# Kernel optimization log

Hardware: AMD Instinct MI355X
Metric: run time of the kernel (lower is better)

## Reference

```python
import jax, jax.numpy as jnp
import numpy as np

B = 8192      # batch
F = 20        # sparse features
V = 1000      # vocab per sparse feature
E = 32        # embedding dim
ND = 10       # dense features
IN0 = (F + ND) * E  # 960 total embed dim
T = 2         # tasks
K = 4         # task experts per task
S = 4         # shared experts
D = 512       # expert dim
H = 256       # tower hidden
TEMP = 2.0    # gate temperature
EPS = 1e-5    # batchnorm eps


def setup_inputs() -> dict:
    key = jax.random.key(0)
    ks = iter(jax.random.split(key, 64))
    n = lambda shape, s=0.02: jax.random.normal(next(ks), shape, dtype=jnp.float32) * s
    inp = {
        'sparse_features': jax.random.randint(next(ks), (B, F), 0, V, dtype=jnp.int32),
        'dense_features': jax.random.normal(next(ks), (B, ND), dtype=jnp.float32),
        'emb_tables': n((F, V, E), 0.05),
        'dense_W': n((ND, ND * E)),
        'dense_b': jnp.zeros((ND * E,), jnp.float32),
    }
    for i, ind in enumerate([IN0, D, D]):
        inp[f'l{i}_Wt'] = n((T, K, ind, D))
        inp[f'l{i}_bt'] = jnp.zeros((T, K, D), jnp.float32)
        inp[f'l{i}_Ws'] = n((S, ind, D))
        inp[f'l{i}_bs'] = jnp.zeros((S, D), jnp.float32)
        inp[f'l{i}_Wg'] = n((T, ind, K + S))
        inp[f'l{i}_bg'] = jnp.zeros((T, K + S), jnp.float32)
    inp['tw1'] = n((T, D, H)); inp['tb1'] = jnp.zeros((T, H), jnp.float32)
    inp['bn_g'] = jnp.ones((T, H), jnp.float32); inp['bn_b'] = jnp.zeros((T, H), jnp.float32)
    inp['bn_m'] = jnp.zeros((T, H), jnp.float32); inp['bn_v'] = jnp.ones((T, H), jnp.float32)
    inp['tw2'] = n((T, H, H // 2)); inp['tb2'] = jnp.zeros((T, H // 2), jnp.float32)
    inp['tw3'] = n((T, H // 2)); inp['tb3'] = jnp.zeros((T,), jnp.float32)
    return inp


def _ple_layer(x, Wt, bt, Ws, bs, Wg, bg):
    # x: [B, in]; Wt: [T,K,in,D]; Ws: [S,in,D]; Wg: [T,in,K+S]
    shared = jax.nn.relu(jnp.einsum('bi,sio->bso', x, Ws) + bs)        # [B,S,D]
    task = jax.nn.relu(jnp.einsum('bi,tkio->btko', x, Wt) + bt)        # [B,T,K,D]
    Bn = x.shape[0]
    stack = jnp.concatenate(
        [task, jnp.broadcast_to(shared[:, None], (Bn, T) + shared.shape[1:])], axis=2)  # [B,T,K+S,D]
    gw = jax.nn.softmax((jnp.einsum('bi,tie->bte', x, Wg) + bg) / TEMP, axis=-1)        # [B,T,K+S]
    return jnp.einsum('bte,bted->btd', gw, stack)                      # [B,T,D]


def reference(sparse_features, dense_features, emb_tables, dense_W, dense_b,
              l0_Wt, l0_bt, l0_Ws, l0_bs, l0_Wg, l0_bg,
              l1_Wt, l1_bt, l1_Ws, l1_bs, l1_Wg, l1_bg,
              l2_Wt, l2_bt, l2_Ws, l2_bs, l2_Wg, l2_bg,
              tw1, tb1, bn_g, bn_b, bn_m, bn_v, tw2, tb2, tw3, tb3):
    # embedding: per-feature table lookup then concat with projected dense
    sp = emb_tables[jnp.arange(F)[None, :], sparse_features]           # [B,F,E]
    embed = jnp.concatenate(
        [sp.reshape(sp.shape[0], F * E), dense_features @ dense_W + dense_b], axis=1)  # [B,IN0]

    x = embed
    tout = None
    for (Wt, bt, Ws, bs, Wg, bg) in [
        (l0_Wt, l0_bt, l0_Ws, l0_bs, l0_Wg, l0_bg),
        (l1_Wt, l1_bt, l1_Ws, l1_bs, l1_Wg, l1_bg),
        (l2_Wt, l2_bt, l2_Ws, l2_bs, l2_Wg, l2_bg),
    ]:
        tout = _ple_layer(x, Wt, bt, Ws, bs, Wg, bg)   # [B,T,D]
        x = tout.mean(axis=1)                           # next layer input

    # task towers (eval mode: BN uses running stats, dropout off)
    h = jnp.einsum('btd,tdh->bth', tout, tw1) + tb1
    h = (h - bn_m) / jnp.sqrt(bn_v + EPS) * bn_g + bn_b
    h = jax.nn.relu(h)
    h = jax.nn.relu(jnp.einsum('bth,thg->btg', h, tw2) + tb2)
    logits = jnp.einsum('btg,tg->bt', h, tw3) + tb3     # [B,T]

    ctr = jax.nn.sigmoid(logits[:, 0])
    cvr_raw = jax.nn.sigmoid(logits[:, 1])
    ctcvr = ctr * cvr_raw
    # use_esmm=True -> cvr_pred == ctcvr
    return jnp.stack([ctr, ctcvr, ctcvr])               # [3,B]: ctr, cvr, ctcvr
```

## Files before the change

kernel.cpp:

```cpp
#include <hip/hip_runtime.h>
#include <math.h>

#define Bn 8192
#define INP0 960
#define Dn 512
#define Hn 256
#define TEMP_INV 0.5f

typedef __attribute__((ext_vector_type(8))) short short8;
typedef __attribute__((ext_vector_type(8))) unsigned short ushort8;
typedef __attribute__((ext_vector_type(4))) float f32x4;
typedef __attribute__((ext_vector_type(2))) long lx2;

__device__ __forceinline__ int swz(int x) { return x ^ ((x >> 3) & 0x70); }

__device__ __forceinline__ unsigned short f2bf(float f) {
  unsigned u = __builtin_bit_cast(unsigned, f);
  u += 0x7FFF + ((u >> 16) & 1);
  return (unsigned short)(u >> 16);
}
__device__ __forceinline__ float bf2f(unsigned short s) {
  unsigned u = ((unsigned)s) << 16;
  return __builtin_bit_cast(float, u);
}
__device__ __forceinline__ int pk4fp8(float a, float b, float c, float d) {
  int r = __builtin_amdgcn_cvt_pk_fp8_f32(a, b, 0, 0);
  r = __builtin_amdgcn_cvt_pk_fp8_f32(c, d, r, 1);
  return r;
}
__device__ __forceinline__ void gload16(const void* g, void* l) {
  __builtin_amdgcn_global_load_lds(
      (const __attribute__((address_space(1))) unsigned int*)g,
      (__attribute__((address_space(3))) unsigned int*)l, 16, 0, 0);
}

#define WBT_L1_OFF 5898240
#define WBT_L2_OFF 9043968

__global__ __launch_bounds__(256) void conv_w_all(
    const float* __restrict__ Wt0, const float* __restrict__ Ws0,
    const float* __restrict__ Wt1, const float* __restrict__ Ws1,
    const float* __restrict__ Wt2, const float* __restrict__ Ws2,
    unsigned char* __restrict__ Wbt) {
  __shared__ float T[64][65];
  int layer = blockIdx.z / 12, e = blockIdx.z - layer * 12;
  int IN = (layer == 0) ? 960 : 512;
  int NK = IN / 64;
  int kk = blockIdx.x;
  if (kk >= NK) return;
  int dblk = blockIdx.y;
  const float* Wtl = (layer == 0) ? Wt0 : (layer == 1) ? Wt1 : Wt2;
  const float* Wsl = (layer == 0) ? Ws0 : (layer == 1) ? Ws1 : Ws2;
  size_t obase = (layer == 0) ? 0 : (layer == 1) ? (size_t)WBT_L1_OFF : (size_t)WBT_L2_OFF;
  int t = threadIdx.x;
  const float* base = (e < 8) ? (Wtl + (size_t)e * IN * Dn) : (Wsl + (size_t)(e - 8) * IN * Dn);
  int k = t >> 2, dg = t & 3;
  const float* gp = base + (size_t)(kk * 64 + k) * Dn + dblk * 64 + dg * 16;
#pragma unroll
  for (int i = 0; i < 4; ++i) {
    float4 v = *(const float4*)(gp + i * 4);
    T[dg * 16 + i * 4 + 0][k] = v.x;
    T[dg * 16 + i * 4 + 1][k] = v.y;
    T[dg * 16 + i * 4 + 2][k] = v.z;
    T[dg * 16 + i * 4 + 3][k] = v.w;
  }
  __syncthreads();
  int col = t >> 2, gq = t & 3;
  int g = gq ^ ((col >> 1) & 3);
  const float* Tc = T[col];
  int4 o;
  o.x = pk4fp8(Tc[g * 8 + 0] * 16.f, Tc[g * 8 + 1] * 16.f, Tc[g * 8 + 2] * 16.f, Tc[g * 8 + 3] * 16.f);
  o.y = pk4fp8(Tc[g * 8 + 4] * 16.f, Tc[g * 8 + 5] * 16.f, Tc[g * 8 + 6] * 16.f, Tc[g * 8 + 7] * 16.f);
  o.z = pk4fp8(Tc[32 + g * 8 + 0] * 16.f, Tc[32 + g * 8 + 1] * 16.f, Tc[32 + g * 8 + 2] * 16.f, Tc[32 + g * 8 + 3] * 16.f);
  o.w = pk4fp8(Tc[32 + g * 8 + 4] * 16.f, Tc[32 + g * 8 + 5] * 16.f, Tc[32 + g * 8 + 6] * 16.f, Tc[32 + g * 8 + 7] * 16.f);
  *(int4*)(Wbt + obase + (((size_t)(dblk * NK + kk) * 12 + e) << 12) + t * 16) = o;
}

__global__ __launch_bounds__(64) void conv_wg_all(
    const float* __restrict__ Wg0, const float* __restrict__ Wg1,
    const float* __restrict__ Wg2, unsigned short* __restrict__ out) {
  int layer = blockIdx.z;
  int IN = (layer == 0) ? 960 : 512;
  int i = blockIdx.x * 64 + threadIdx.x;
  if (i >= IN) return;
  int e = blockIdx.y;
  int t = e >> 3, eg = e & 7;
  const float* Wg = (layer == 0) ? Wg0 : (layer == 1) ? Wg1 : Wg2;
  size_t off = (layer == 0) ? 0 : (layer == 1) ? (size_t)16 * 960 : (size_t)16 * 960 + 16 * 512;
  out[off + (size_t)e * IN + i] = f2bf(Wg[((size_t)t * IN + i) * 8 + eg]);
}

template <int K, int H>
__global__ __launch_bounds__(256) void conv_tw(const float* __restrict__ W,
                                               unsigned short* __restrict__ out) {
  __shared__ float T[64][33];
  int kk = blockIdx.x, hb = blockIdx.y, t = blockIdx.z;
  int tid = threadIdx.x;
  const float* base = W + (size_t)t * K * H;
  int k = tid >> 3, dq = tid & 7;
  const float* gp = base + (size_t)(kk * 32 + k) * H + hb * 64 + dq * 8;
  float4 v0 = *(const float4*)gp, v1 = *(const float4*)(gp + 4);
  T[dq * 8 + 0][k] = v0.x; T[dq * 8 + 1][k] = v0.y; T[dq * 8 + 2][k] = v0.z; T[dq * 8 + 3][k] = v0.w;
  T[dq * 8 + 4][k] = v1.x; T[dq * 8 + 5][k] = v1.y; T[dq * 8 + 6][k] = v1.z; T[dq * 8 + 7][k] = v1.w;
  __syncthreads();
  int L = tid * 16;
  int nat = swz(L);
  int c = nat >> 6, k0 = (nat & 63) >> 1;
  ushort8 o;
#pragma unroll
  for (int u = 0; u < 8; ++u) o[u] = f2bf(T[c][k0 + u]);
  const int NHB = H / 64;
  *(ushort8*)(out + (((size_t)(kk * NHB + hb) * 2 + t) << 11) + (L >> 1)) = o;
}

__global__ __launch_bounds__(256) void embed_kernel(
    const int* __restrict__ sparse, const float* __restrict__ dense,
    const float* __restrict__ emb, const float* __restrict__ dW,
    const float* __restrict__ db, const unsigned short* __restrict__ wgb0,
    const float* __restrict__ bg0,
    unsigned short* __restrict__ xn, unsigned char* __restrict__ xt,
    float* __restrict__ gates) {
  int b0 = blockIdx.x * 4, t = threadIdx.x;
  __shared__ float dfs[4][10];
  __shared__ __align__(16) unsigned short xrow[4][960];
  if (t < 40) dfs[t / 10][t % 10] = dense[(b0 + t / 10) * 10 + t % 10];
  __syncthreads();
  if (t < 240) {
    int c = t * 4;
#pragma unroll 1
    for (int r = 0; r < 4; ++r) {
      int b = b0 + r;
      float v[4];
      if (c < 640) {
        int f = c >> 5, e0 = c & 31;
        int idx = sparse[b * 20 + f];
        const float* ep = emb + ((size_t)f * 1000 + idx) * 32 + e0;
        float4 q = *(const float4*)ep;
        v[0] = q.x; v[1] = q.y; v[2] = q.z; v[3] = q.w;
      } else {
        int j = c - 640;
#pragma unroll
        for (int u = 0; u < 4; ++u) {
          float a = db[j + u];
#pragma unroll
          for (int d = 0; d < 10; ++d) a += dfs[r][d] * dW[d * 320 + j + u];
          v[u] = a;
        }
      }
      ushort4 pk;
      pk.x = f2bf(v[0]); pk.y = f2bf(v[1]); pk.z = f2bf(v[2]); pk.w = f2bf(v[3]);
      *(ushort4*)(xn + (size_t)b * 960 + c) = pk;
      *(ushort4*)(&xrow[r][c]) = pk;
      int col = b & 63;
      int lc = c & 63;
      int ks = lc >> 5, g = (lc & 31) >> 3, j0 = lc & 7;
      int gq = g ^ ((col >> 1) & 3);
      int pos = (col << 6) + (gq << 4) + (ks << 3) + j0;
      int p8 = pk4fp8(v[0] * 16.f, v[1] * 16.f, v[2] * 16.f, v[3] * 16.f);
      *(int*)(xt + (((size_t)(c >> 6) * 128 + (b >> 6)) << 12) + pos) = p8;
    }
  }
  __syncthreads();
  int r = t >> 6, lane = t & 63;
  int e = lane & 15, slice = lane >> 4;
  const unsigned short* xr = &xrow[r][slice * 240];
  const unsigned short* wr = wgb0 + (size_t)e * 960 + slice * 240;
  float p = 0.f;
#pragma unroll 2
  for (int i = 0; i < 240; i += 8) {
    short8 xv = *(const short8*)(xr + i);
    short8 wv2 = *(const short8*)(wr + i);
#pragma unroll
    for (int u = 0; u < 8; ++u)
      p += bf2f((unsigned short)xv[u]) * bf2f((unsigned short)wv2[u]);
  }
  p += __shfl_xor(p, 16);
  p += __shfl_xor(p, 32);
  float z = (p + bg0[e]) * TEMP_INV;
  float m = z;
  m = fmaxf(m, __shfl_xor(m, 1)); m = fmaxf(m, __shfl_xor(m, 2)); m = fmaxf(m, __shfl_xor(m, 4));
  float ex = expf(z - m);
  float s = ex;
  s += __shfl_xor(s, 1); s += __shfl_xor(s, 2); s += __shfl_xor(s, 4);
  if (lane < 16) gates[(size_t)(b0 + r) * 16 + lane] = ex / s;
}

template <int IN>
__global__ __launch_bounds__(256) void gate_kernel(
    const unsigned short* __restrict__ x, const unsigned short* __restrict__ wgb,
    const float* __restrict__ bg, float* __restrict__ gates) {
  int tid = threadIdx.x;
  int wv = tid >> 6, lane = tid & 63;
  int b = blockIdx.x * 4 + wv;
  int e = lane & 15, slice = lane >> 4;
  const unsigned short* xr = x + (size_t)b * IN + slice * (IN / 4);
  const unsigned short* wr = wgb + (size_t)e * IN + slice * (IN / 4);
  float p = 0.f;
#pragma unroll 2
  for (int i = 0; i < IN / 4; i += 8) {
    short8 xv = *(const short8*)(xr + i);
    short8 wv2 = *(const short8*)(wr + i);
#pragma unroll
    for (int u = 0; u < 8; ++u)
      p += bf2f((unsigned short)xv[u]) * bf2f((unsigned short)wv2[u]);
  }
  p += __shfl_xor(p, 16);
  p += __shfl_xor(p, 32);
  int t = e >> 3, eg = e & 7;
  float z = (p + bg[t * 8 + eg]) * TEMP_INV;
  float m = z;
  m = fmaxf(m, __shfl_xor(m, 1)); m = fmaxf(m, __shfl_xor(m, 2)); m = fmaxf(m, __shfl_xor(m, 4));
  float ex = expf(z - m);
  float s = ex;
  s += __shfl_xor(s, 1); s += __shfl_xor(s, 2); s += __shfl_xor(s, 4);
  if (lane < 16) gates[(size_t)b * 16 + lane] = ex / s;
}

#define GSH 0
#define OUTS 4096
#define SB 22528
#define STG 53248

template <int IN, int MODE>
__global__ __launch_bounds__(768, 3) void ple_mfma(
    const unsigned char* __restrict__ xt, const float* __restrict__ gates,
    const unsigned char* __restrict__ Wbt,
    const float* __restrict__ btb, const float* __restrict__ bsh,
    unsigned short* __restrict__ outn, unsigned char* __restrict__ outt8,
    unsigned short* __restrict__ outtb) {
  __shared__ __align__(16) char smem[129024];
  const int NK = IN / 64;
  int tid = threadIdx.x;
  int wv = tid >> 6, lane = tid & 63;
  int r = lane & 15, g = lane >> 4;
  int s = blockIdx.x;
  int dblk = s & 7, bblk = s >> 3;
  int b0 = bblk * 64, d0 = dblk * 64;

  if (tid < 256)
    *(float4*)(smem + GSH + tid * 16) = *(const float4*)(gates + (size_t)b0 * 16 + tid * 4);

  f32x4 acc[4][4];
#pragma unroll
  for (int i = 0; i < 4; ++i)
#pragma unroll
    for (int j = 0; j < 4; ++j) acc[i][j] = f32x4{0.f, 0.f, 0.f, 0.f};

  const unsigned char* xchunk = xt + ((size_t)bblk << 12);
  const unsigned char* wchunk = Wbt + (size_t)(dblk * NK) * 49152;

  auto stage = [&](int t, char* lb) {
    const unsigned char* ws = wchunk + (size_t)t * 49152;
#pragma unroll
    for (int i = 0; i < 4; ++i)
      gload16(ws + tid * 16 + i * 12288, lb + tid * 16 + i * 12288);
    if (tid < 256)
      gload16(xchunk + (size_t)t * (128 * 4096) + tid * 16, lb + 49152 + tid * 16);
  };

  stage(0, smem + SB);

  for (int kk = 0; kk < NK; ++kk) {
    asm volatile("s_waitcnt vmcnt(0)" ::: "memory");
    __builtin_amdgcn_s_barrier();
    if (kk + 1 < NK) stage(kk + 1, smem + SB + ((kk + 1) & 1) * STG);
    {
      const char* lb = smem + SB + (kk & 1) * STG;
      const char* xb = lb + 49152;
      const char* wb = lb + (wv << 12);
      int base = (r << 6) + ((g ^ ((r >> 1) & 3)) << 4);
      lx2 A[4], B[4];
#pragma unroll
      for (int rt = 0; rt < 4; ++rt) A[rt] = *(const lx2*)(xb + rt * 1024 + base);
#pragma unroll
      for (int ct = 0; ct < 4; ++ct) B[ct] = *(const lx2*)(wb + ct * 1024 + base);
#pragma unroll
      for (int rt = 0; rt < 4; ++rt)
#pragma unroll
        for (int ct = 0; ct < 4; ++ct)
          acc[rt][ct] = __builtin_amdgcn_mfma_f32_16x16x32_fp8_fp8(A[rt][0], B[ct][0], acc[rt][ct], 0, 0, 0);
#pragma unroll
      for (int rt = 0; rt < 4; ++rt)
#pragma unroll
        for (int ct = 0; ct < 4; ++ct)
          acc[rt][ct] = __builtin_amdgcn_mfma_f32_16x16x32_fp8_fp8(A[rt][1], B[ct][1], acc[rt][ct], 0, 0, 0);
    }
  }
  __syncthreads();

  {
    const float* bp = (wv < 8) ? (btb + wv * Dn) : (bsh + (wv - 8) * Dn);
    float bias[4];
#pragma unroll
    for (int ct = 0; ct < 4; ++ct) bias[ct] = bp[d0 + ct * 16 + r];
    char* ex = smem + SB + (wv << 12);
#pragma unroll
    for (int rt = 0; rt < 4; ++rt)
#pragma unroll
      for (int ct = 0; ct < 4; ++ct) {
        float v0 = fmaxf(acc[rt][ct][0] * 0.00390625f + bias[ct], 0.f) * 16.f;
        float v1 = fmaxf(acc[rt][ct][1] * 0.00390625f + bias[ct], 0.f) * 16.f;
        float v2 = fmaxf(acc[rt][ct][2] * 0.00390625f + bias[ct], 0.f) * 16.f;
        float v3 = fmaxf(acc[rt][ct][3] * 0.00390625f + bias[ct], 0.f) * 16.f;
        int col = ct * 16 + r;
        int off = (col << 6) + rt * 16 + g * 4;
        off ^= (col & 7) << 3;
        *(int*)(ex + off) = pk4fp8(v0, v1, v2, v3);
      }
  }
  __syncthreads();

  if (tid < 512) {
    int col = tid & 63, q = tid >> 6;
    int exoff = ((col << 6) + (q << 3)) ^ ((col & 7) << 3);
    long v[12];
#pragma unroll
    for (int e = 0; e < 12; ++e)
      v[e] = *(const long*)(smem + SB + (e << 12) + exoff);
    unsigned short* os0 = (unsigned short*)(smem + OUTS);
    unsigned short* os1 = os0 + 64 * 72;
#pragma unroll
    for (int half = 0; half < 2; ++half) {
#pragma unroll
      for (int jj = 0; jj < 4; ++jj) {
        int row = (q << 3) + half * 4 + jj;
        const float* gp = (const float*)(smem + GSH + (row << 6));
        float4 ga = ((const float4*)gp)[0];
        float4 gb = ((const float4*)gp)[1];
        float4 gc = ((const float4*)gp)[2];
        float4 gd = ((const float4*)gp)[3];
        float f[12];
#pragma unroll
        for (int e = 0; e < 12; ++e) {
          unsigned w32 = (unsigned)(v[e] >> (half * 32));
          f[e] = __builtin_amdgcn_cvt_f32_fp8((int)(w32 >> (jj * 8)), 0);
        }
        float s0 = ga.x * f[0] + ga.y * f[1] + ga.z * f[2] + ga.w * f[3] +
                   gb.x * f[8] + gb.y * f[9] + gb.z * f[10] + gb.w * f[11];
        float s1 = gc.x * f[4] + gc.y * f[5] + gc.z * f[6] + gc.w * f[7] +
                   gd.x * f[8] + gd.y * f[9] + gd.z * f[10] + gd.w * f[11];
        os0[row * 72 + col] = f2bf(s0 * 0.0625f);
        os1[row * 72 + col] = f2bf(s1 * 0.0625f);
      }
    }
  }
  __syncthreads();

  if (tid < 512) {
    int row = tid >> 3, cq = tid & 7;
    const unsigned short* os0 = (const unsigned short*)(smem + OUTS) + row * 72 + cq * 8;
    const unsigned short* os1 = os0 + 64 * 72;
    ushort8 p0 = *(const ushort8*)os0, p1 = *(const ushort8*)os1;
    int b = b0 + row, d = d0 + cq * 8;
    if (MODE == 0) {
      float m[8];
      ushort8 pk;
#pragma unroll
      for (int u = 0; u < 8; ++u) {
        m[u] = 0.5f * (bf2f((unsigned short)p0[u]) + bf2f((unsigned short)p1[u]));
        pk[u] = f2bf(m[u]);
      }
      *(ushort8*)(outn + (size_t)b * Dn + d) = pk;
      int lk = d & 63;
      int ks = lk >> 5, g2 = (lk & 31) >> 3;
      int gq = g2 ^ ((row >> 1) & 3);
      int pos = (row << 6) + (gq << 4) + (ks << 3);
      int2 o8;
      o8.x = pk4fp8(m[0] * 16.f, m[1] * 16.f, m[2] * 16.f, m[3] * 16.f);
      o8.y = pk4fp8(m[4] * 16.f, m[5] * 16.f, m[6] * 16.f, m[7] * 16.f);
      *(int2*)(outt8 + (((size_t)dblk * 128 + bblk) << 12) + pos) = o8;
    } else {
      int kk2 = d >> 5;
      int nat = (row << 6) + ((d & 31) << 1);
      *(ushort8*)(outtb + (((size_t)(0 * 16 + kk2) * 128 + bblk) << 11) + (swz(nat) >> 1)) = p0;
      *(ushort8*)(outtb + (((size_t)(1 * 16 + kk2) * 128 + bblk) << 11) + (swz(nat) >> 1)) = p1;
    }
  }
}

#define TWBUF 36864
#define H1OFF 73728

__global__ __launch_bounds__(512) void tower_mfma(
    const unsigned short* __restrict__ toutT,
    const unsigned short* __restrict__ twbt1, const unsigned short* __restrict__ twbt2,
    const float* __restrict__ tb1,
    const float* __restrict__ bng, const float* __restrict__ bnb,
    const float* __restrict__ bnm, const float* __restrict__ bnv,
    const float* __restrict__ tb2, const float* __restrict__ tw3,
    const float* __restrict__ tb3, float* __restrict__ out) {
  __shared__ __align__(16) char smem[106496];
  int tid = threadIdx.x;
  int wv = tid >> 6, lane = tid & 63, r = lane & 15, g = lane >> 4;
  int blk = blockIdx.x;
  int bblk = blk >> 1, sub = blk & 1;
  int b0 = blk * 32;
  char* h1t = smem + H1OFF;

  int t1 = wv >> 2, hb = wv & 3;
  f32x4 acc[2][4];
#pragma unroll
  for (int i = 0; i < 2; ++i)
#pragma unroll
    for (int j = 0; j < 4; ++j) acc[i][j] = f32x4{0.f, 0.f, 0.f, 0.f};

  auto stage1 = [&](int t, char* lb) {
#pragma unroll
    for (int i = 0; i < 4; ++i)
      gload16((const char*)twbt1 + (size_t)t * 32768 + tid * 16 + i * 8192,
              lb + tid * 16 + i * 8192);
    if (tid < 256) {
      int tt = tid >> 7, off = (tid & 127) * 16;
      gload16((const char*)toutT + (((size_t)(tt * 16 + t) * 128 + bblk) << 12) + sub * 2048 + off,
              lb + 32768 + tt * 2048 + off);
    }
  };

  stage1(0, smem);
  __syncthreads();
  int cur = 0;
  for (int kk = 0; kk < 16; ++kk) {
    if (kk + 1 < 16) stage1(kk + 1, smem + (cur ^ 1) * TWBUF);
    {
      const char* lb = smem + cur * TWBUF;
      const char* wb = lb + (hb * 2 + t1) * 4096;
      const char* xb = lb + 32768 + t1 * 2048;
      short8 a[2], bfr[4];
#pragma unroll
      for (int rt = 0; rt < 2; ++rt)
        a[rt] = *(const short8*)(xb + swz(((rt * 16 + r) << 6) + (g << 4)));
#pragma unroll
      for (int ct = 0; ct < 4; ++ct)
        bfr[ct] = *(const short8*)(wb + swz(((ct * 16 + r) << 6) + (g << 4)));
#pragma unroll
      for (int rt = 0; rt < 2; ++rt)
#pragma unroll
        for (int ct = 0; ct < 4; ++ct)
          acc[rt][ct] = __builtin_amdgcn_mfma_f32_16x16x32_bf16(a[rt], bfr[ct], acc[rt][ct], 0, 0, 0);
    }
    __syncthreads();
    cur ^= 1;
  }

  {
#pragma unroll
    for (int ct = 0; ct < 4; ++ct) {
      int h = hb * 64 + ct * 16 + r;
      int idx = t1 * 256 + h;
      float inv = rsqrtf(bnv[idx] + 1e-5f) * bng[idx];
      float mu = bnm[idx], be = bnb[idx], bias = tb1[idx];
      int kk2 = h >> 5, kloc = h & 31;
      char* tile = h1t + (t1 * 8 + kk2) * 2048;
#pragma unroll
      for (int rt = 0; rt < 2; ++rt)
#pragma unroll
        for (int j = 0; j < 4; ++j) {
          int lr = rt * 16 + g * 4 + j;
          float v = acc[rt][ct][j] + bias;
          v = (v - mu) * inv + be;
          v = fmaxf(v, 0.f);
          *(unsigned short*)(tile + swz((lr << 6) + (kloc << 1))) = f2bf(v);
        }
    }
  }
  __syncthreads();

  float* h2x = (float*)smem;
  if (wv < 4) {
    int t2 = wv >> 1, hb2 = wv & 1;
    f32x4 acc2[2][4];
#pragma unroll
    for (int i = 0; i < 2; ++i)
#pragma unroll
      for (int j = 0; j < 4; ++j) acc2[i][j] = f32x4{0.f, 0.f, 0.f, 0.f};
    for (int kk = 0; kk < 8; ++kk) {
      const char* xb = h1t + (t2 * 8 + kk) * 2048;
      const char* wb = (const char*)twbt2 + ((kk * 2 + hb2) * 2 + t2) * 4096;
      short8 a[2], bfr[4];
#pragma unroll
      for (int rt = 0; rt < 2; ++rt)
        a[rt] = *(const short8*)(xb + swz(((rt * 16 + r) << 6) + (g << 4)));
#pragma unroll
      for (int ct = 0; ct < 4; ++ct)
        bfr[ct] = *(const short8*)(wb + swz(((ct * 16 + r) << 6) + (g << 4)));
#pragma unroll
      for (int rt = 0; rt < 2; ++rt)
#pragma unroll
        for (int ct = 0; ct < 4; ++ct)
          acc2[rt][ct] = __builtin_amdgcn_mfma_f32_16x16x32_bf16(a[rt], bfr[ct], acc2[rt][ct], 0, 0, 0);
    }
#pragma unroll
    for (int ct = 0; ct < 4; ++ct) {
      int col = hb2 * 64 + ct * 16 + r;
      float bias = tb2[t2 * 128 + col];
#pragma unroll
      for (int rt = 0; rt < 2; ++rt)
#pragma unroll
        for (int j = 0; j < 4; ++j) {
          int lr = rt * 16 + g * 4 + j;
          h2x[(t2 * 32 + lr) * 129 + col] = fmaxf(acc2[rt][ct][j] + bias, 0.f);
        }
    }
  }
  __syncthreads();

  float* lgs = (float*)(smem + 40960);
  if (tid < 64) {
    int t3 = tid >> 5, lr = tid & 31;
    const float* hr = h2x + (t3 * 32 + lr) * 129;
    const float* w3 = tw3 + t3 * 128;
    float s = 0.f;
#pragma unroll 8
    for (int i = 0; i < 128; ++i) s += hr[i] * w3[i];
    lgs[t3 * 32 + lr] = s + tb3[t3];
  }
  __syncthreads();
  if (tid < 32) {
    int b = b0 + tid;
    float ctr = 1.f / (1.f + expf(-lgs[tid]));
    float cvr = 1.f / (1.f + expf(-lgs[32 + tid]));
    float cc = ctr * cvr;
    out[b] = ctr;
    out[Bn + b] = cc;
    out[2 * Bn + b] = cc;
  }
}

extern "C" void kernel_launch(void* const* d_in, const int* in_sizes, int n_in,
                              void* d_out, int out_size, void* d_ws, size_t ws_size,
                              hipStream_t stream) {
  const int* sparse   = (const int*)d_in[0];
  const float* dense  = (const float*)d_in[1];
  const float* emb    = (const float*)d_in[2];
  const float* dW     = (const float*)d_in[3];
  const float* db     = (const float*)d_in[4];
  const float* Wt[3]  = {(const float*)d_in[5],  (const float*)d_in[11], (const float*)d_in[17]};
  const float* btb[3] = {(const float*)d_in[6],  (const float*)d_in[12], (const float*)d_in[18]};
  const float* Wsh[3] = {(const float*)d_in[7],  (const float*)d_in[13], (const float*)d_in[19]};
  const float* bsh[3] = {(const float*)d_in[8],  (const float*)d_in[14], (const float*)d_in[20]};
  const float* Wg[3]  = {(const float*)d_in[9],  (const float*)d_in[15], (const float*)d_in[21]};
  const float* bg[3]  = {(const float*)d_in[10], (const float*)d_in[16], (const float*)d_in[22]};
  const float* tw1 = (const float*)d_in[23];
  const float* tb1 = (const float*)d_in[24];
  const float* bng = (const float*)d_in[25];
  const float* bnb = (const float*)d_in[26];
  const float* bnm = (const float*)d_in[27];
  const float* bnv = (const float*)d_in[28];
  const float* tw2 = (const float*)d_in[29];
  const float* tb2 = (const float*)d_in[30];
  const float* tw3 = (const float*)d_in[31];
  const float* tb3 = (const float*)d_in[32];

  unsigned short* x0n = (unsigned short*)d_ws;
  unsigned short* x1n = x0n + (size_t)Bn * 960;
  unsigned short* toutT = x1n + (size_t)Bn * 512;
  float* gatesB = (float*)(toutT + (size_t)Bn * 1024);
  unsigned short* twbt1 = (unsigned short*)(gatesB + (size_t)Bn * 16);
  unsigned short* twbt2 = twbt1 + (size_t)2 * 512 * 256;
  unsigned char* x0t = (unsigned char*)(twbt2 + (size_t)2 * 256 * 128);
  unsigned char* x1t = x0t + (size_t)Bn * 960;
  unsigned char* Wbt = x1t + (size_t)Bn * 512;
  unsigned short* wgb = (unsigned short*)(Wbt + (size_t)12189696);
  unsigned short* wgb0 = wgb;
  unsigned short* wgb1 = wgb0 + (size_t)16 * 960;
  unsigned short* wgb2 = wgb1 + (size_t)16 * 512;
  unsigned short* x2n = x0n;
  unsigned char* x2t = x0t;

  conv_tw<512, 256><<<dim3(16, 4, 2), 256, 0, stream>>>(tw1, twbt1);
  conv_tw<256, 128><<<dim3(8, 2, 2), 256, 0, stream>>>(tw2, twbt2);
  conv_wg_all<<<dim3(15, 16, 3), 64, 0, stream>>>(Wg[0], Wg[1], Wg[2], wgb);
  conv_w_all<<<dim3(15, 8, 36), 256, 0, stream>>>(Wt[0], Wsh[0], Wt[1], Wsh[1],
                                                  Wt[2], Wsh[2], Wbt);

  embed_kernel<<<Bn / 4, 256, 0, stream>>>(sparse, dense, emb, dW, db, wgb0, bg[0],
                                           x0n, x0t, gatesB);
  ple_mfma<960, 0><<<1024, 768, 0, stream>>>(x0t, gatesB, Wbt, btb[0], bsh[0], x1n, x1t, nullptr);

  gate_kernel<512><<<Bn / 4, 256, 0, stream>>>(x1n, wgb1, bg[1], gatesB);
  ple_mfma<512, 0><<<1024, 768, 0, stream>>>(x1t, gatesB, Wbt + WBT_L1_OFF, btb[1], bsh[1],
                                             x2n, x2t, nullptr);

  gate_kernel<512><<<Bn / 4, 256, 0, stream>>>(x2n, wgb2, bg[2], gatesB);
  ple_mfma<512, 1><<<1024, 768, 0, stream>>>(x2t, gatesB, Wbt + WBT_L2_OFF, btb[2], bsh[2],
                                             nullptr, nullptr, toutT);

  tower_mfma<<<256, 512, 0, stream>>>(toutT, twbt1, twbt2, tb1, bng, bnb, bnm, bnv,
                                      tb2, tw3, tb3, (float*)d_out);
}
```

Measured before the change: 294.6 us.

## Use 16x16x128 scaled FP8 MFMA with three-buffer pipeline and padded K

Replaces pairs of 16x16x32 FP8 MFMAs with the gfx950 scaled 16x16x128 f8f6f4 MFMA. Each instruction consumes two 64-wide K chunks, fed by an even and an odd staged buffer. Layer 0's K is zero-padded from 15 to 16 chunks in both the weight and activation buffers, and staging becomes a 3-slot ring buffer with two chunks in flight. The aim is fewer MFMA issues and better load/compute overlap. The cost is extra padding writes, more LDS (3 stages), and an added barrier per iteration.

```diff
diff --git a/kernel.cpp b/kernel.cpp
--- a/kernel.cpp
+++ b/kernel.cpp
@@ -2,7 +2,6 @@
 #include <math.h>
 
 #define Bn 8192
-#define INP0 960
 #define Dn 512
 #define Hn 256
 #define TEMP_INV 0.5f
@@ -10,7 +9,8 @@
 typedef __attribute__((ext_vector_type(8))) short short8;
 typedef __attribute__((ext_vector_type(8))) unsigned short ushort8;
 typedef __attribute__((ext_vector_type(4))) float f32x4;
-typedef __attribute__((ext_vector_type(2))) long lx2;
+typedef __attribute__((ext_vector_type(4))) int iv4;
+typedef __attribute__((ext_vector_type(8))) int iv8;
 
 __device__ __forceinline__ int swz(int x) { return x ^ ((x >> 3) & 0x70); }
 
@@ -34,8 +34,8 @@
       (__attribute__((address_space(3))) unsigned int*)l, 16, 0, 0);
 }
 
-#define WBT_L1_OFF 5898240
-#define WBT_L2_OFF 9043968
+#define WBT_L1_OFF 6291456
+#define WBT_L2_OFF 9437184
 
 __global__ __launch_bounds__(256) void conv_w_all(
     const float* __restrict__ Wt0, const float* __restrict__ Ws0,
@@ -46,13 +46,20 @@
   int layer = blockIdx.z / 12, e = blockIdx.z - layer * 12;
   int IN = (layer == 0) ? 960 : 512;
   int NK = IN / 64;
+  int NKP = (layer == 0) ? 16 : 8;
   int kk = blockIdx.x;
-  if (kk >= NK) return;
   int dblk = blockIdx.y;
+  size_t obase = (layer == 0) ? 0 : (layer == 1) ? (size_t)WBT_L1_OFF : (size_t)WBT_L2_OFF;
+  int t = threadIdx.x;
+  if (kk >= NK) {
+    if (layer == 0 && kk == 15) {
+      iv4 z = {0, 0, 0, 0};
+      *(iv4*)(Wbt + obase + (((size_t)(dblk * NKP + 15) * 12 + e) << 12) + t * 16) = z;
+    }
+    return;
+  }
   const float* Wtl = (layer == 0) ? Wt0 : (layer == 1) ? Wt1 : Wt2;
   const float* Wsl = (layer == 0) ? Ws0 : (layer == 1) ? Ws1 : Ws2;
-  size_t obase = (layer == 0) ? 0 : (layer == 1) ? (size_t)WBT_L1_OFF : (size_t)WBT_L2_OFF;
-  int t = threadIdx.x;
   const float* base = (e < 8) ? (Wtl + (size_t)e * IN * Dn) : (Wsl + (size_t)(e - 8) * IN * Dn);
   int k = t >> 2, dg = t & 3;
   const float* gp = base + (size_t)(kk * 64 + k) * Dn + dblk * 64 + dg * 16;
@@ -73,7 +80,7 @@
   o.y = pk4fp8(Tc[g * 8 + 4] * 16.f, Tc[g * 8 + 5] * 16.f, Tc[g * 8 + 6] * 16.f, Tc[g * 8 + 7] * 16.f);
   o.z = pk4fp8(Tc[32 + g * 8 + 0] * 16.f, Tc[32 + g * 8 + 1] * 16.f, Tc[32 + g * 8 + 2] * 16.f, Tc[32 + g * 8 + 3] * 16.f);
   o.w = pk4fp8(Tc[32 + g * 8 + 4] * 16.f, Tc[32 + g * 8 + 5] * 16.f, Tc[32 + g * 8 + 6] * 16.f, Tc[32 + g * 8 + 7] * 16.f);
-  *(int4*)(Wbt + obase + (((size_t)(dblk * NK + kk) * 12 + e) << 12) + t * 16) = o;
+  *(int4*)(Wbt + obase + (((size_t)(dblk * NKP + kk) * 12 + e) << 12) + t * 16) = o;
 }
 
 __global__ __launch_bounds__(64) void conv_wg_all(
@@ -160,6 +167,12 @@
       *(int*)(xt + (((size_t)(c >> 6) * 128 + (b >> 6)) << 12) + pos) = p8;
     }
   }
+  if (t < 16) {
+    int rr = t >> 2, ch = t & 3;
+    int b = b0 + rr;
+    iv4 z = {0, 0, 0, 0};
+    *(iv4*)(xt + (((size_t)(15 * 128 + (b >> 6))) << 12) + (b & 63) * 64 + ch * 16) = z;
+  }
   __syncthreads();
   int r = t >> 6, lane = t & 63;
   int e = lane & 15, slice = lane >> 4;
@@ -216,20 +229,16 @@
   if (lane < 16) gates[(size_t)b * 16 + lane] = ex / s;
 }
 
-#define GSH 0
-#define OUTS 4096
-#define SB 22528
 #define STG 53248
 
-template <int IN, int MODE>
+template <int NKP, int MODE>
 __global__ __launch_bounds__(768, 3) void ple_mfma(
     const unsigned char* __restrict__ xt, const float* __restrict__ gates,
     const unsigned char* __restrict__ Wbt,
     const float* __restrict__ btb, const float* __restrict__ bsh,
     unsigned short* __restrict__ outn, unsigned char* __restrict__ outt8,
     unsigned short* __restrict__ outtb) {
-  __shared__ __align__(16) char smem[129024];
-  const int NK = IN / 64;
+  __shared__ __align__(16) char smem[3 * STG];
   int tid = threadIdx.x;
   int wv = tid >> 6, lane = tid & 63;
   int r = lane & 15, g = lane >> 4;
@@ -237,9 +246,6 @@
   int dblk = s & 7, bblk = s >> 3;
   int b0 = bblk * 64, d0 = dblk * 64;
 
-  if (tid < 256)
-    *(float4*)(smem + GSH + tid * 16) = *(const float4*)(gates + (size_t)b0 * 16 + tid * 4);
-
   f32x4 acc[4][4];
 #pragma unroll
   for (int i = 0; i < 4; ++i)
@@ -247,7 +253,7 @@
     for (int j = 0; j < 4; ++j) acc[i][j] = f32x4{0.f, 0.f, 0.f, 0.f};
 
   const unsigned char* xchunk = xt + ((size_t)bblk << 12);
-  const unsigned char* wchunk = Wbt + (size_t)(dblk * NK) * 49152;
+  const unsigned char* wchunk = Wbt + (size_t)dblk * NKP * 49152;
 
   auto stage = [&](int t, char* lb) {
     const unsigned char* ws = wchunk + (size_t)t * 49152;
@@ -258,42 +264,54 @@
       gload16(xchunk + (size_t)t * (128 * 4096) + tid * 16, lb + 49152 + tid * 16);
   };
 
-  stage(0, smem + SB);
-
-  for (int kk = 0; kk < NK; ++kk) {
+  const int NS = NKP / 2;
+  stage(0, smem);
+  stage(1, smem + STG);
+
+  for (int i = 0; i < NS; ++i) {
+    if (i > 0) stage(2 * i + 1, smem + ((2 * i + 1) % 3) * STG);
     asm volatile("s_waitcnt vmcnt(0)" ::: "memory");
     __builtin_amdgcn_s_barrier();
-    if (kk + 1 < NK) stage(kk + 1, smem + SB + ((kk + 1) & 1) * STG);
+    if (2 * i + 2 < NKP) stage(2 * i + 2, smem + ((2 * i + 2) % 3) * STG);
     {
-      const char* lb = smem + SB + (kk & 1) * STG;
-      const char* xb = lb + 49152;
-      const char* wb = lb + (wv << 12);
+      const char* lbE = smem + ((2 * i) % 3) * STG;
+      const char* lbO = smem + ((2 * i + 1) % 3) * STG;
+      const char* xbE = lbE + 49152;
+      const char* xbO = lbO + 49152;
+      const char* wbE = lbE + (wv << 12);
+      const char* wbO = lbO + (wv << 12);
       int base = (r << 6) + ((g ^ ((r >> 1) & 3)) << 4);
-      lx2 A[4], B[4];
-#pragma unroll
-      for (int rt = 0; rt < 4; ++rt) A[rt] = *(const lx2*)(xb + rt * 1024 + base);
-#pragma unroll
-      for (int ct = 0; ct < 4; ++ct) B[ct] = *(const lx2*)(wb + ct * 1024 + base);
-#pragma unroll
-      for (int rt = 0; rt < 4; ++rt)
-#pragma unroll
-        for (int ct = 0; ct < 4; ++ct)
-          acc[rt][ct] = __builtin_amdgcn_mfma_f32_16x16x32_fp8_fp8(A[rt][0], B[ct][0], acc[rt][ct], 0, 0, 0);
-#pragma unroll
-      for (int rt = 0; rt < 4; ++rt)
-#pragma unroll
-        for (int ct = 0; ct < 4; ++ct)
-          acc[rt][ct] = __builtin_amdgcn_mfma_f32_16x16x32_fp8_fp8(A[rt][1], B[ct][1], acc[rt][ct], 0, 0, 0);
-    }
-  }
-  __syncthreads();
+      iv8 A[4];
+#pragma unroll
+      for (int rt = 0; rt < 4; ++rt) {
+        iv4 lo = *(const iv4*)(xbE + rt * 1024 + base);
+        iv4 hi = *(const iv4*)(xbO + rt * 1024 + base);
+        A[rt] = __builtin_shufflevector(lo, hi, 0, 1, 2, 3, 4, 5, 6, 7);
+      }
+#pragma unroll
+      for (int ct = 0; ct < 4; ++ct) {
+        iv4 lo = *(const iv4*)(wbE + ct * 1024 + base);
+        iv4 hi = *(const iv4*)(wbO + ct * 1024 + base);
+        iv8 Bf = __builtin_shufflevector(lo, hi, 0, 1, 2, 3, 4, 5, 6, 7);
+#pragma unroll
+        for (int rt = 0; rt < 4; ++rt)
+          acc[rt][ct] = __builtin_amdgcn_mfma_scale_f32_16x16x128_f8f6f4(
+              A[rt], Bf, acc[rt][ct], 0, 0, 0, 127, 0, 127);
+      }
+    }
+    __builtin_amdgcn_s_barrier();
+  }
+  __syncthreads();
+
+  if (tid < 256)
+    *(float4*)(smem + 2 * STG + tid * 16) = *(const float4*)(gates + (size_t)b0 * 16 + tid * 4);
 
   {
     const float* bp = (wv < 8) ? (btb + wv * Dn) : (bsh + (wv - 8) * Dn);
     float bias[4];
 #pragma unroll
     for (int ct = 0; ct < 4; ++ct) bias[ct] = bp[d0 + ct * 16 + r];
-    char* ex = smem + SB + (wv << 12);
+    char* ex = smem + (wv << 12);
 #pragma unroll
     for (int rt = 0; rt < 4; ++rt)
 #pragma unroll
@@ -316,15 +334,15 @@
     long v[12];
 #pragma unroll
     for (int e = 0; e < 12; ++e)
-      v[e] = *(const long*)(smem + SB + (e << 12) + exoff);
-    unsigned short* os0 = (unsigned short*)(smem + OUTS);
+      v[e] = *(const long*)(smem + (e << 12) + exoff);
+    unsigned short* os0 = (unsigned short*)(smem + STG);
     unsigned short* os1 = os0 + 64 * 72;
 #pragma unroll
     for (int half = 0; half < 2; ++half) {
 #pragma unroll
       for (int jj = 0; jj < 4; ++jj) {
         int row = (q << 3) + half * 4 + jj;
-        const float* gp = (const float*)(smem + GSH + (row << 6));
+        const float* gp = (const float*)(smem + 2 * STG + (row << 6));
         float4 ga = ((const float4*)gp)[0];
         float4 gb = ((const float4*)gp)[1];
         float4 gc = ((const float4*)gp)[2];
@@ -348,7 +366,7 @@
 
   if (tid < 512) {
     int row = tid >> 3, cq = tid & 7;
-    const unsigned short* os0 = (const unsigned short*)(smem + OUTS) + row * 72 + cq * 8;
+    const unsigned short* os0 = (const unsigned short*)(smem + STG) + row * 72 + cq * 8;
     const unsigned short* os1 = os0 + 64 * 72;
     ushort8 p0 = *(const ushort8*)os0, p1 = *(const ushort8*)os1;
     int b = b0 + row, d = d0 + cq * 8;
@@ -558,9 +576,9 @@
   unsigned short* twbt1 = (unsigned short*)(gatesB + (size_t)Bn * 16);
   unsigned short* twbt2 = twbt1 + (size_t)2 * 512 * 256;
   unsigned char* x0t = (unsigned char*)(twbt2 + (size_t)2 * 256 * 128);
-  unsigned char* x1t = x0t + (size_t)Bn * 960;
+  unsigned char* x1t = x0t + (size_t)Bn * 1024;
   unsigned char* Wbt = x1t + (size_t)Bn * 512;
-  unsigned short* wgb = (unsigned short*)(Wbt + (size_t)12189696);
+  unsigned short* wgb = (unsigned short*)(Wbt + (size_t)12582912);
   unsigned short* wgb0 = wgb;
   unsigned short* wgb1 = wgb0 + (size_t)16 * 960;
   unsigned short* wgb2 = wgb1 + (size_t)16 * 512;
@@ -570,20 +588,20 @@
   conv_tw<512, 256><<<dim3(16, 4, 2), 256, 0, stream>>>(tw1, twbt1);
   conv_tw<256, 128><<<dim3(8, 2, 2), 256, 0, stream>>>(tw2, twbt2);
   conv_wg_all<<<dim3(15, 16, 3), 64, 0, stream>>>(Wg[0], Wg[1], Wg[2], wgb);
-  conv_w_all<<<dim3(15, 8, 36), 256, 0, stream>>>(Wt[0], Wsh[0], Wt[1], Wsh[1],
+  conv_w_all<<<dim3(16, 8, 36), 256, 0, stream>>>(Wt[0], Wsh[0], Wt[1], Wsh[1],
                                                   Wt[2], Wsh[2], Wbt);
 
   embed_kernel<<<Bn / 4, 256, 0, stream>>>(sparse, dense, emb, dW, db, wgb0, bg[0],
                                            x0n, x0t, gatesB);
-  ple_mfma<960, 0><<<1024, 768, 0, stream>>>(x0t, gatesB, Wbt, btb[0], bsh[0], x1n, x1t, nullptr);
+  ple_mfma<16, 0><<<1024, 768, 0, stream>>>(x0t, gatesB, Wbt, btb[0], bsh[0], x1n, x1t, nullptr);
 
   gate_kernel<512><<<Bn / 4, 256, 0, stream>>>(x1n, wgb1, bg[1], gatesB);
-  ple_mfma<512, 0><<<1024, 768, 0, stream>>>(x1t, gatesB, Wbt + WBT_L1_OFF, btb[1], bsh[1],
-                                             x2n, x2t, nullptr);
+  ple_mfma<8, 0><<<1024, 768, 0, stream>>>(x1t, gatesB, Wbt + WBT_L1_OFF, btb[1], bsh[1],
+                                           x2n, x2t, nullptr);
 
   gate_kernel<512><<<Bn / 4, 256, 0, stream>>>(x2n, wgb2, bg[2], gatesB);
-  ple_mfma<512, 1><<<1024, 768, 0, stream>>>(x2t, gatesB, Wbt + WBT_L2_OFF, btb[2], bsh[2],
-                                             nullptr, nullptr, toutT);
+  ple_mfma<8, 1><<<1024, 768, 0, stream>>>(x2t, gatesB, Wbt + WBT_L2_OFF, btb[2], bsh[2],
+                                           nullptr, nullptr, toutT);
 
   tower_mfma<<<256, 512, 0, stream>>>(toutT, twbt1, twbt2, tb1, bng, bnb, bnm, bnv,
                                       tb2, tw3, tb3, (float*)d_out);
```

Result: slower. 472.2 us (+60.3%).

## Load weight fragments directly into registers and triple-buffer activations in LDS

Applied to the files above, without the earlier changes.

The main GEMM loop no longer stages the 48KB weight tile through shared memory. Each wave now loads its own pre-swizzled weight fragments straight from global memory into double-buffered registers, while only the activation tile goes through a three-slot LDS ring with a two-step prefetch and split vmcnt waits. This removes LDS write/read traffic for weights and cuts shared memory from about 126KB to 78KB, which could allow more blocks per CU. The cost is extra VGPRs for the prefetched fragments and a fully unrolled K loop. Global latency now also sits directly in front of the MFMAs, with no LDS staging in between.

```diff
diff --git a/kernel.cpp b/kernel.cpp
--- a/kernel.cpp
+++ b/kernel.cpp
@@ -216,10 +216,9 @@
   if (lane < 16) gates[(size_t)b * 16 + lane] = ex / s;
 }
 
-#define GSH 0
-#define OUTS 4096
-#define SB 22528
-#define STG 53248
+#define XR 4096
+#define EXO 12288
+#define OUTS 61440
 
 template <int IN, int MODE>
 __global__ __launch_bounds__(768, 3) void ple_mfma(
@@ -228,7 +227,7 @@
     const float* __restrict__ btb, const float* __restrict__ bsh,
     unsigned short* __restrict__ outn, unsigned char* __restrict__ outt8,
     unsigned short* __restrict__ outtb) {
-  __shared__ __align__(16) char smem[129024];
+  __shared__ __align__(16) char smem[79872];
   const int NK = IN / 64;
   int tid = threadIdx.x;
   int wv = tid >> 6, lane = tid & 63;
@@ -236,64 +235,74 @@
   int s = blockIdx.x;
   int dblk = s & 7, bblk = s >> 3;
   int b0 = bblk * 64, d0 = dblk * 64;
+  bool stager = (tid < 256);
+
+  f32x4 acc[4][4];
+#pragma unroll
+  for (int i = 0; i < 4; ++i)
+#pragma unroll
+    for (int j = 0; j < 4; ++j) acc[i][j] = f32x4{0.f, 0.f, 0.f, 0.f};
+
+  const unsigned char* xchunk = xt + ((size_t)bblk << 12);
+  int base = (r << 6) + ((g ^ ((r >> 1) & 3)) << 4);
+  const unsigned char* wtile = Wbt + (size_t)(dblk * NK) * 49152 + (wv << 12) + base;
+
+  auto stage_x = [&](int t) {
+    if (stager)
+      gload16(xchunk + (size_t)t * (128 * 4096) + tid * 16, smem + (t % 3) * XR + tid * 16);
+  };
+
+  lx2 Bpre[2][4];
+#pragma unroll
+  for (int ct = 0; ct < 4; ++ct) Bpre[0][ct] = *(const lx2*)(wtile + ct * 1024);
+  stage_x(0);
+  stage_x(1);
+
+#pragma unroll
+  for (int kk = 0; kk < NK; ++kk) {
+    if (kk + 1 < NK) {
+      if (stager) asm volatile("s_waitcnt vmcnt(1)" ::: "memory");
+      else        asm volatile("s_waitcnt vmcnt(0)" ::: "memory");
+    } else {
+      asm volatile("s_waitcnt vmcnt(0)" ::: "memory");
+    }
+    __builtin_amdgcn_s_barrier();
+    if (kk + 1 < NK) {
+      const unsigned char* wt = wtile + (size_t)(kk + 1) * 49152;
+#pragma unroll
+      for (int ct = 0; ct < 4; ++ct) Bpre[(kk + 1) & 1][ct] = *(const lx2*)(wt + ct * 1024);
+    }
+    if (kk + 2 < NK) stage_x(kk + 2);
+    {
+      const char* xb = smem + (kk % 3) * XR;
+      lx2 A[4];
+#pragma unroll
+      for (int rt = 0; rt < 4; ++rt) A[rt] = *(const lx2*)(xb + rt * 1024 + base);
+#pragma unroll
+      for (int rt = 0; rt < 4; ++rt)
+#pragma unroll
+        for (int ct = 0; ct < 4; ++ct)
+          acc[rt][ct] = __builtin_amdgcn_mfma_f32_16x16x32_fp8_fp8(
+              A[rt][0], Bpre[kk & 1][ct][0], acc[rt][ct], 0, 0, 0);
+#pragma unroll
+      for (int rt = 0; rt < 4; ++rt)
+#pragma unroll
+        for (int ct = 0; ct < 4; ++ct)
+          acc[rt][ct] = __builtin_amdgcn_mfma_f32_16x16x32_fp8_fp8(
+              A[rt][1], Bpre[kk & 1][ct][1], acc[rt][ct], 0, 0, 0);
+    }
+  }
+  __syncthreads();
 
   if (tid < 256)
-    *(float4*)(smem + GSH + tid * 16) = *(const float4*)(gates + (size_t)b0 * 16 + tid * 4);
-
-  f32x4 acc[4][4];
-#pragma unroll
-  for (int i = 0; i < 4; ++i)
-#pragma unroll
-    for (int j = 0; j < 4; ++j) acc[i][j] = f32x4{0.f, 0.f, 0.f, 0.f};
-
-  const unsigned char* xchunk = xt + ((size_t)bblk << 12);
-  const unsigned char* wchunk = Wbt + (size_t)(dblk * NK) * 49152;
-
-  auto stage = [&](int t, char* lb) {
-    const unsigned char* ws = wchunk + (size_t)t * 49152;
-#pragma unroll
-    for (int i = 0; i < 4; ++i)
-      gload16(ws + tid * 16 + i * 12288, lb + tid * 16 + i * 12288);
-    if (tid < 256)
-      gload16(xchunk + (size_t)t * (128 * 4096) + tid * 16, lb + 49152 + tid * 16);
-  };
-
-  stage(0, smem + SB);
-
-  for (int kk = 0; kk < NK; ++kk) {
-    asm volatile("s_waitcnt vmcnt(0)" ::: "memory");
-    __builtin_amdgcn_s_barrier();
-    if (kk + 1 < NK) stage(kk + 1, smem + SB + ((kk + 1) & 1) * STG);
-    {
-      const char* lb = smem + SB + (kk & 1) * STG;
-      const char* xb = lb + 49152;
-      const char* wb = lb + (wv << 12);
-      int base = (r << 6) + ((g ^ ((r >> 1) & 3)) << 4);
-      lx2 A[4], B[4];
-#pragma unroll
-      for (int rt = 0; rt < 4; ++rt) A[rt] = *(const lx2*)(xb + rt * 1024 + base);
-#pragma unroll
-      for (int ct = 0; ct < 4; ++ct) B[ct] = *(const lx2*)(wb + ct * 1024 + base);
-#pragma unroll
-      for (int rt = 0; rt < 4; ++rt)
-#pragma unroll
-        for (int ct = 0; ct < 4; ++ct)
-          acc[rt][ct] = __builtin_amdgcn_mfma_f32_16x16x32_fp8_fp8(A[rt][0], B[ct][0], acc[rt][ct], 0, 0, 0);
-#pragma unroll
-      for (int rt = 0; rt < 4; ++rt)
-#pragma unroll
-        for (int ct = 0; ct < 4; ++ct)
-          acc[rt][ct] = __builtin_amdgcn_mfma_f32_16x16x32_fp8_fp8(A[rt][1], B[ct][1], acc[rt][ct], 0, 0, 0);
-    }
-  }
-  __syncthreads();
+    *(float4*)(smem + tid * 16) = *(const float4*)(gates + (size_t)b0 * 16 + tid * 4);
 
   {
     const float* bp = (wv < 8) ? (btb + wv * Dn) : (bsh + (wv - 8) * Dn);
     float bias[4];
 #pragma unroll
     for (int ct = 0; ct < 4; ++ct) bias[ct] = bp[d0 + ct * 16 + r];
-    char* ex = smem + SB + (wv << 12);
+    char* ex = smem + EXO + (wv << 12);
 #pragma unroll
     for (int rt = 0; rt < 4; ++rt)
 #pragma unroll
@@ -316,7 +325,7 @@
     long v[12];
 #pragma unroll
     for (int e = 0; e < 12; ++e)
-      v[e] = *(const long*)(smem + SB + (e << 12) + exoff);
+      v[e] = *(const long*)(smem + EXO + (e << 12) + exoff);
     unsigned short* os0 = (unsigned short*)(smem + OUTS);
     unsigned short* os1 = os0 + 64 * 72;
 #pragma unroll
@@ -324,7 +333,7 @@
 #pragma unroll
       for (int jj = 0; jj < 4; ++jj) {
         int row = (q << 3) + half * 4 + jj;
-        const float* gp = (const float*)(smem + GSH + (row << 6));
+        const float* gp = (const float*)(smem + (row << 6));
         float4 ga = ((const float4*)gp)[0];
         float4 gb = ((const float4*)gp)[1];
         float4 gc = ((const float4*)gp)[2];
```

Result: slower. 306.6 us (+4.1%).

## Single-buffer PLE stage tiles to shrink LDS and raise occupancy

Applied to the files above, without the earlier changes.

Replaces the double-buffered weight/activation staging in the PLE MFMA kernel with a single LDS buffer that is refilled after each k-step's compute and barrier. The gate tile and output staging are moved and the epilogue runs in two halves of 32 rows on 256 threads, so LDS use drops from about 126KB to about 61KB and launch bounds ask for 6 waves per SIMD instead of 3. The aim is to fit two workgroups per CU so one block's loads hide behind another's MFMAs. In exchange, each block now serializes its own loads and compute, and the epilogue adds a barrier while using fewer threads.

```diff
diff --git a/kernel.cpp b/kernel.cpp
--- a/kernel.cpp
+++ b/kernel.cpp
@@ -216,19 +216,17 @@
   if (lane < 16) gates[(size_t)b * 16 + lane] = ex / s;
 }
 
-#define GSH 0
-#define OUTS 4096
-#define SB 22528
-#define STG 53248
+#define GTS 49152
+#define OUTS 53248
 
 template <int IN, int MODE>
-__global__ __launch_bounds__(768, 3) void ple_mfma(
+__global__ __launch_bounds__(768, 6) void ple_mfma(
     const unsigned char* __restrict__ xt, const float* __restrict__ gates,
     const unsigned char* __restrict__ Wbt,
     const float* __restrict__ btb, const float* __restrict__ bsh,
     unsigned short* __restrict__ outn, unsigned char* __restrict__ outt8,
     unsigned short* __restrict__ outtb) {
-  __shared__ __align__(16) char smem[129024];
+  __shared__ __align__(16) char smem[62464];
   const int NK = IN / 64;
   int tid = threadIdx.x;
   int wv = tid >> 6, lane = tid & 63;
@@ -237,9 +235,6 @@
   int dblk = s & 7, bblk = s >> 3;
   int b0 = bblk * 64, d0 = dblk * 64;
 
-  if (tid < 256)
-    *(float4*)(smem + GSH + tid * 16) = *(const float4*)(gates + (size_t)b0 * 16 + tid * 4);
-
   f32x4 acc[4][4];
 #pragma unroll
   for (int i = 0; i < 4; ++i)
@@ -249,25 +244,23 @@
   const unsigned char* xchunk = xt + ((size_t)bblk << 12);
   const unsigned char* wchunk = Wbt + (size_t)(dblk * NK) * 49152;
 
-  auto stage = [&](int t, char* lb) {
+  auto stage = [&](int t) {
     const unsigned char* ws = wchunk + (size_t)t * 49152;
 #pragma unroll
     for (int i = 0; i < 4; ++i)
-      gload16(ws + tid * 16 + i * 12288, lb + tid * 16 + i * 12288);
+      gload16(ws + tid * 16 + i * 12288, smem + tid * 16 + i * 12288);
     if (tid < 256)
-      gload16(xchunk + (size_t)t * (128 * 4096) + tid * 16, lb + 49152 + tid * 16);
+      gload16(xchunk + (size_t)t * (128 * 4096) + tid * 16, smem + GTS + tid * 16);
   };
 
-  stage(0, smem + SB);
+  stage(0);
 
   for (int kk = 0; kk < NK; ++kk) {
     asm volatile("s_waitcnt vmcnt(0)" ::: "memory");
     __builtin_amdgcn_s_barrier();
-    if (kk + 1 < NK) stage(kk + 1, smem + SB + ((kk + 1) & 1) * STG);
     {
-      const char* lb = smem + SB + (kk & 1) * STG;
-      const char* xb = lb + 49152;
-      const char* wb = lb + (wv << 12);
+      const char* xb = smem + GTS;
+      const char* wb = smem + (wv << 12);
       int base = (r << 6) + ((g ^ ((r >> 1) & 3)) << 4);
       lx2 A[4], B[4];
 #pragma unroll
@@ -285,15 +278,20 @@
         for (int ct = 0; ct < 4; ++ct)
           acc[rt][ct] = __builtin_amdgcn_mfma_f32_16x16x32_fp8_fp8(A[rt][1], B[ct][1], acc[rt][ct], 0, 0, 0);
     }
-  }
-  __syncthreads();
+    __syncthreads();
+    if (kk + 1 < NK) stage(kk + 1);
+  }
+  __syncthreads();
+
+  if (tid < 256)
+    *(float4*)(smem + GTS + tid * 16) = *(const float4*)(gates + (size_t)b0 * 16 + tid * 4);
 
   {
     const float* bp = (wv < 8) ? (btb + wv * Dn) : (bsh + (wv - 8) * Dn);
     float bias[4];
 #pragma unroll
     for (int ct = 0; ct < 4; ++ct) bias[ct] = bp[d0 + ct * 16 + r];
-    char* ex = smem + SB + (wv << 12);
+    char* ex = smem + (wv << 12);
 #pragma unroll
     for (int rt = 0; rt < 4; ++rt)
 #pragma unroll
@@ -310,70 +308,76 @@
   }
   __syncthreads();
 
-  if (tid < 512) {
-    int col = tid & 63, q = tid >> 6;
-    int exoff = ((col << 6) + (q << 3)) ^ ((col & 7) << 3);
-    long v[12];
-#pragma unroll
-    for (int e = 0; e < 12; ++e)
-      v[e] = *(const long*)(smem + SB + (e << 12) + exoff);
-    unsigned short* os0 = (unsigned short*)(smem + OUTS);
-    unsigned short* os1 = os0 + 64 * 72;
-#pragma unroll
-    for (int half = 0; half < 2; ++half) {
-#pragma unroll
-      for (int jj = 0; jj < 4; ++jj) {
-        int row = (q << 3) + half * 4 + jj;
-        const float* gp = (const float*)(smem + GSH + (row << 6));
-        float4 ga = ((const float4*)gp)[0];
-        float4 gb = ((const float4*)gp)[1];
-        float4 gc = ((const float4*)gp)[2];
-        float4 gd = ((const float4*)gp)[3];
-        float f[12];
-#pragma unroll
-        for (int e = 0; e < 12; ++e) {
-          unsigned w32 = (unsigned)(v[e] >> (half * 32));
-          f[e] = __builtin_amdgcn_cvt_f32_fp8((int)(w32 >> (jj * 8)), 0);
+  unsigned short* os0 = (unsigned short*)(smem + OUTS);
+  unsigned short* os1 = os0 + 32 * 72;
+#pragma unroll
+  for (int h = 0; h < 2; ++h) {
+    if (h) __syncthreads();
+    if (tid < 256) {
+      int col = tid & 63, qq = tid >> 6;
+      int q = h * 4 + qq;
+      int exoff = ((col << 6) + (q << 3)) ^ ((col & 7) << 3);
+      long v[12];
+#pragma unroll
+      for (int e = 0; e < 12; ++e)
+        v[e] = *(const long*)(smem + (e << 12) + exoff);
+#pragma unroll
+      for (int half = 0; half < 2; ++half) {
+#pragma unroll
+        for (int jj = 0; jj < 4; ++jj) {
+          int row = (q << 3) + half * 4 + jj;
+          int rl = row - h * 32;
+          const float* gp = (const float*)(smem + GTS + (row << 6));
+          float4 ga = ((const float4*)gp)[0];
+          float4 gb = ((const float4*)gp)[1];
+          float4 gc = ((const float4*)gp)[2];
+          float4 gd = ((const float4*)gp)[3];
+          float f[12];
+#pragma unroll
+          for (int e = 0; e < 12; ++e) {
+            unsigned w32 = (unsigned)(v[e] >> (half * 32));
+            f[e] = __builtin_amdgcn_cvt_f32_fp8((int)(w32 >> (jj * 8)), 0);
+          }
+          float s0 = ga.x * f[0] + ga.y * f[1] + ga.z * f[2] + ga.w * f[3] +
+                     gb.x * f[8] + gb.y * f[9] + gb.z * f[10] + gb.w * f[11];
+          float s1 = gc.x * f[4] + gc.y * f[5] + gc.z * f[6] + gc.w * f[7] +
+                     gd.x * f[8] + gd.y * f[9] + gd.z * f[10] + gd.w * f[11];
+          os0[rl * 72 + col] = f2bf(s0 * 0.0625f);
+          os1[rl * 72 + col] = f2bf(s1 * 0.0625f);
         }
-        float s0 = ga.x * f[0] + ga.y * f[1] + ga.z * f[2] + ga.w * f[3] +
-                   gb.x * f[8] + gb.y * f[9] + gb.z * f[10] + gb.w * f[11];
-        float s1 = gc.x * f[4] + gc.y * f[5] + gc.z * f[6] + gc.w * f[7] +
-                   gd.x * f[8] + gd.y * f[9] + gd.z * f[10] + gd.w * f[11];
-        os0[row * 72 + col] = f2bf(s0 * 0.0625f);
-        os1[row * 72 + col] = f2bf(s1 * 0.0625f);
       }
     }
-  }
-  __syncthreads();
-
-  if (tid < 512) {
-    int row = tid >> 3, cq = tid & 7;
-    const unsigned short* os0 = (const unsigned short*)(smem + OUTS) + row * 72 + cq * 8;
-    const unsigned short* os1 = os0 + 64 * 72;
-    ushort8 p0 = *(const ushort8*)os0, p1 = *(const ushort8*)os1;
-    int b = b0 + row, d = d0 + cq * 8;
-    if (MODE == 0) {
-      float m[8];
-      ushort8 pk;
-#pragma unroll
-      for (int u = 0; u < 8; ++u) {
-        m[u] = 0.5f * (bf2f((unsigned short)p0[u]) + bf2f((unsigned short)p1[u]));
-        pk[u] = f2bf(m[u]);
+    __syncthreads();
+    if (tid < 256) {
+      int rl = tid >> 3, cq = tid & 7;
+      const unsigned short* p0p = os0 + rl * 72 + cq * 8;
+      const unsigned short* p1p = os1 + rl * 72 + cq * 8;
+      ushort8 p0 = *(const ushort8*)p0p, p1 = *(const ushort8*)p1p;
+      int row = h * 32 + rl;
+      int b = b0 + row, d = d0 + cq * 8;
+      if (MODE == 0) {
+        float m[8];
+        ushort8 pk;
+#pragma unroll
+        for (int u = 0; u < 8; ++u) {
+          m[u] = 0.5f * (bf2f((unsigned short)p0[u]) + bf2f((unsigned short)p1[u]));
+          pk[u] = f2bf(m[u]);
+        }
+        *(ushort8*)(outn + (size_t)b * Dn + d) = pk;
+        int lk = d & 63;
+        int ks = lk >> 5, g2 = (lk & 31) >> 3;
+        int gq = g2 ^ ((row >> 1) & 3);
+        int pos = (row << 6) + (gq << 4) + (ks << 3);
+        int2 o8;
+        o8.x = pk4fp8(m[0] * 16.f, m[1] * 16.f, m[2] * 16.f, m[3] * 16.f);
+        o8.y = pk4fp8(m[4] * 16.f, m[5] * 16.f, m[6] * 16.f, m[7] * 16.f);
+        *(int2*)(outt8 + (((size_t)dblk * 128 + bblk) << 12) + pos) = o8;
+      } else {
+        int kk2 = d >> 5;
+        int nat = (row << 6) + ((d & 31) << 1);
+        *(ushort8*)(outtb + (((size_t)(0 * 16 + kk2) * 128 + bblk) << 11) + (swz(nat) >> 1)) = p0;
+        *(ushort8*)(outtb + (((size_t)(1 * 16 + kk2) * 128 + bblk) << 11) + (swz(nat) >> 1)) = p1;
       }
-      *(ushort8*)(outn + (size_t)b * Dn + d) = pk;
-      int lk = d & 63;
-      int ks = lk >> 5, g2 = (lk & 31) >> 3;
-      int gq = g2 ^ ((row >> 1) & 3);
-      int pos = (row << 6) + (gq << 4) + (ks << 3);
-      int2 o8;
-      o8.x = pk4fp8(m[0] * 16.f, m[1] * 16.f, m[2] * 16.f, m[3] * 16.f);
-      o8.y = pk4fp8(m[4] * 16.f, m[5] * 16.f, m[6] * 16.f, m[7] * 16.f);
-      *(int2*)(outt8 + (((size_t)dblk * 128 + bblk) << 12) + pos) = o8;
-    } else {
-      int kk2 = d >> 5;
-      int nat = (row << 6) + ((d & 31) << 1);
-      *(ushort8*)(outtb + (((size_t)(0 * 16 + kk2) * 128 + bblk) << 11) + (swz(nat) >> 1)) = p0;
-      *(ushort8*)(outtb + (((size_t)(1 * 16 + kk2) * 128 + bblk) << 11) + (swz(nat) >> 1)) = p1;
     }
   }
 }
```

Result: slower. 608.7 us (+106.6%).
